# Optimization experiments

Measured on AMD Instinct MI355X. Metric: run time of the kernel, lower is better.

## Reference

```python
import jax, jax.numpy as jnp
import numpy as np

AGENT, WIN = 6, 7

def _rel_pos_index(d, h, w):
    # same construction as the torch buffer `relative_position_index`
    coords = np.stack(np.meshgrid(np.arange(d), np.arange(h), np.arange(w), indexing='ij'))
    cf = coords.reshape(3, -1)                                   # [3, S]
    rc = (cf[:, :, None] - cf[:, None, :]).transpose(1, 2, 0).astype(np.int64)
    rc[:, :, 0] += d - 1; rc[:, :, 1] += h - 1; rc[:, :, 2] += w - 1
    rc[:, :, 0] *= (2 * h - 1) * (2 * w - 1)
    rc[:, :, 1] *= (2 * w - 1)
    return jnp.asarray(rc.sum(-1))                               # [S, S]

def setup_inputs() -> dict:
    key = jax.random.key(0)
    ks = jax.random.split(key, 11)
    b, L, X, Y, w1, w2, dim = 2, AGENT, 8, 8, WIN, WIN, 256
    heads, ch, nt = 8, 32, 2
    table = (2 * L - 1) * (2 * w1 - 1) * (2 * w2 - 1)
    f = lambda k, s: (0.02 * jax.random.normal(k, s)).astype(jnp.float32)
    return dict(
        x=jax.random.normal(ks[0], (b, L, X, Y, w1, w2, dim), jnp.float32),
        Wq=f(ks[1], (nt, dim, dim)), bq=f(ks[2], (nt, dim)),
        Wk=f(ks[3], (nt, dim, dim)), bk=f(ks[4], (nt, dim)),
        Wv=f(ks[5], (nt, dim, dim)), bv=f(ks[6], (nt, dim)),
        rel_att=f(ks[7], (nt * nt, heads, ch, ch)),
        rel_msg=f(ks[8], (nt * nt, heads, ch, ch)),
        bias_table=f(ks[9], (table, heads)),
        Wo=f(ks[10], (dim, dim)),
        agent_type=1,
    )

def reference(x, Wq, bq, Wk, bk, Wv, bv, rel_att, rel_msg, bias_table, Wo, agent_type):
    b, L, X, Y, w1, w2, dim = x.shape
    heads, ch = rel_att.shape[1], rel_att.shape[2]
    nt = Wq.shape[0]
    scale = ch ** -0.5
    # types = [0] + (agent_size-1)*[type], identical across batch (as in forward)
    types = jnp.concatenate([jnp.zeros(1, jnp.int32),
                             jnp.full((L - 1,), agent_type, jnp.int32)])

    def proj(W, bias):
        # type-indexed per-agent linear (gathered batched matmul instead of python loops)
        y = jnp.einsum('blxyuvd,lde->blxyuve', x, W[types])
        y = y + bias[types][None, :, None, None, None, None, :]
        # -> [b, n=(X*Y) windows, m heads, L agents, p=(w1*w2) tokens, c]
        return y.reshape(b, L, X * Y, w1 * w2, heads, ch).transpose(0, 2, 4, 1, 3, 5)

    q = proj(Wq, bq) * scale
    k = proj(Wk, bk)
    v = proj(Wv, bv)

    # relation weights gathered by (src_type, dst_type) pair: [m, L, L, c, c]
    rel = types[:, None] * nt + types[None, :]
    w_att = rel_att[rel].transpose(2, 0, 1, 3, 4)
    w_msg = rel_msg[rel].transpose(2, 0, 1, 3, 4)

    # bilinear hetero attention scores, grouped by agent pair (i,j)
    sim = jnp.einsum('bnmipc,mijcf,bnmjqf->bnmipjq', q, w_att, k)
    S, n = L * w1 * w2, X * Y
    sim = sim.reshape(b, n, heads, S, S)
    idx = _rel_pos_index(L, w1, w2)                                # [S, S] static
    sim = sim + bias_table[idx].transpose(2, 0, 1)                 # + [m, S, S] rel-pos bias
    attn = jax.nn.softmax(sim, axis=-1).reshape(b, n, heads, L, w1 * w2, L, w1 * w2)

    # relation-transformed messages, then attention-weighted aggregation
    vt = jnp.einsum('mijcf,bnmjqf->bnmijqc', w_msg, v)
    out = jnp.einsum('bnmipjq,bnmijqc->bnmipc', attn, vt)
    # [b, n, m, L, p, c] -> [b, L, X, Y, w1, w2, dim]
    out = out.transpose(0, 3, 1, 4, 2, 5).reshape(b, L, X, Y, w1, w2, dim)
    return out @ Wo.T
```

## Files before the change

kernel.cpp:

```cpp
#include <hip/hip_runtime.h>
#include <hip/hip_bf16.h>

typedef __hip_bfloat16 bf16;
typedef unsigned short u16;
typedef short bf16x8 __attribute__((ext_vector_type(8)));
typedef float f32x4  __attribute__((ext_vector_type(4)));

#define BB    2
#define LL    6
#define NWIN  64
#define PP    49
#define DIMM  256
#define HEADS 8
#define CHN   32
#define SS    294
#define ASTRIDE 264
#define BSTRIDE 304
#define VST 328
#define PST 168

__device__ __forceinline__ u16 bfbits(float x) { return __bfloat16_as_ushort(__float2bfloat16(x)); }
__device__ __forceinline__ f32x4 mfma16(bf16x8 a, bf16x8 b, f32x4 c) {
    return __builtin_amdgcn_mfma_f32_16x16x32_bf16(a, b, c, 0, 0, 0);
}

__global__ __launch_bounds__(256) void k_prep(
    const float* __restrict__ Wq, const float* __restrict__ Wk, const float* __restrict__ Wv,
    const float* __restrict__ Wo, const float* __restrict__ ra, const float* __restrict__ rm,
    const float* __restrict__ bt,
    u16* __restrict__ wT, u16* __restrict__ Wob, u16* __restrict__ raT, u16* __restrict__ rmb,
    float* __restrict__ biasM)
{
    const int blk = blockIdx.x;
    if (blk < 1792) {
        const int idx = blk*256 + threadIdx.x;
        if (idx >= 7*65536) return;
        const int mat = idx >> 16, rem = idx & 65535;
        if (mat < 6) {
            const int tz = mat >> 1, t = mat & 1;
            const int e = rem >> 8, d = rem & 255;
            const float* W = (tz == 0 ? Wq : tz == 1 ? Wk : Wv);
            wT[mat*65536 + rem] = bfbits(W[t*65536 + d*256 + e]);
        } else {
            Wob[rem] = bfbits(Wo[rem]);
        }
    } else if (blk < 1920) {
        const int idx = (blk - 1792)*256 + threadIdx.x;
        if (idx < 4*HEADS*CHN*CHN) {
            const int pm = idx >> 10, cf = idx & 1023, c = cf >> 5, f = cf & 31;
            raT[(pm << 10) + (f << 5) + c] = bfbits(ra[idx]);
            rmb[idx] = bfbits(rm[idx]);
        }
    } else {
        const int idx = (blk - 1920)*256 + threadIdx.x;
        if (idx < HEADS*SS*BSTRIDE) {
            const int m = idx / (SS*BSTRIDE);
            const int rem = idx % (SS*BSTRIDE);
            const int s1 = rem / BSTRIDE, s2 = rem % BSTRIDE;
            float val = 0.f;
            if (s2 < SS) {
                const int i1 = s1/49, p1 = s1 - i1*49, h1 = p1/7, w1 = p1 - h1*7;
                const int j2 = s2/49, p2 = s2 - j2*49, h2 = p2/7, w2 = p2 - h2*7;
                const int rc = i1*169 + h1*13 + w1, cc = j2*169 + h2*13 + w2;
                val = bt[(rc - cc + 929)*8 + m];
            }
            biasM[idx] = val;
        }
    }
}

__global__ __launch_bounds__(256) void k_qkv2(
    const float* __restrict__ x, const u16* __restrict__ wT,
    const float* __restrict__ bq, const float* __restrict__ bk, const float* __restrict__ bv,
    const int* __restrict__ atype,
    u16* __restrict__ q, u16* __restrict__ k, u16* __restrict__ v)
{
    __shared__ __align__(16) u16 As[64*ASTRIDE];
    const int tid = threadIdx.x;
    const int w = tid >> 6, lane = tid & 63;
    const int g4 = lane >> 4, c16 = lane & 15;
    const int bid3 = blockIdx.x;
    const int tz = bid3 % 3;
    const int bid = bid3 / 3;
    const int nwin = bid & 63;
    const int l = (bid >> 6) % LL;
    const int b = bid / (LL*NWIN);

    const float4* xp = (const float4*)(x + (size_t)bid * (PP*DIMM));
    for (int idx = tid; idx < 49*64; idx += 256) {
        const int row = idx >> 6, c4 = idx & 63;
        const float4 xv = xp[idx];
        ushort4 h;
        h.x = bfbits(xv.x); h.y = bfbits(xv.y); h.z = bfbits(xv.z); h.w = bfbits(xv.w);
        *(ushort4*)&As[row*ASTRIDE + c4*4] = h;
    }
    const ushort4 z4 = {0, 0, 0, 0};
    for (int idx = tid; idx < 15*66; idx += 256) {
        const int row = 49 + idx/66, c4 = idx%66;
        *(ushort4*)&As[row*ASTRIDE + c4*4] = z4;
    }
    __syncthreads();

    const int t = (l == 0) ? 0 : atype[0];
    const f32x4 zero4 = {0.f, 0.f, 0.f, 0.f};

    const u16* WT = wT + (size_t)(tz*2 + t)*65536;
    const float* bias = (tz == 0 ? bq : tz == 1 ? bk : bv) + t*DIMM;
    u16* dst = (tz == 0 ? q : tz == 1 ? k : v);
    const float scale = (tz == 0) ? 0.17677669529663687f : 1.0f;

    f32x4 acc[4][4];
    #pragma unroll
    for (int mm = 0; mm < 4; ++mm)
        #pragma unroll
        for (int nn = 0; nn < 4; ++nn) acc[mm][nn] = zero4;

    for (int ks = 0; ks < 8; ++ks) {
        bf16x8 a[4], bb[4];
        #pragma unroll
        for (int mm = 0; mm < 4; ++mm)
            a[mm] = *(const bf16x8*)&As[(mm*16 + c16)*ASTRIDE + ks*32 + g4*8];
        #pragma unroll
        for (int nn = 0; nn < 4; ++nn)
            bb[nn] = *(const bf16x8*)&WT[(size_t)(w*64 + nn*16 + c16)*256 + ks*32 + g4*8];
        #pragma unroll
        for (int mm = 0; mm < 4; ++mm)
            #pragma unroll
            for (int nn = 0; nn < 4; ++nn)
                acc[mm][nn] = mfma16(a[mm], bb[nn], acc[mm][nn]);
    }

    #pragma unroll
    for (int nn = 0; nn < 4; ++nn) {
        const int col = w*64 + nn*16 + c16;
        const float bval = bias[col];
        const int head = col >> 5, c = col & 31;
        const size_t base = (((size_t)(b*NWIN + nwin)*HEADS + head)*SS + l*PP)*CHN + c;
        #pragma unroll
        for (int mm = 0; mm < 4; ++mm) {
            #pragma unroll
            for (int r = 0; r < 4; ++r) {
                const int row = mm*16 + g4*4 + r;
                if (row < PP)
                    dst[base + (size_t)row*CHN] = bfbits((acc[mm][nn][r] + bval)*scale);
            }
        }
    }
}

__global__ __launch_bounds__(256) void k_attn(
    const u16* __restrict__ q, const u16* __restrict__ kk_, const u16* __restrict__ v,
    const u16* __restrict__ raT, const u16* __restrict__ rmb,
    const float* __restrict__ biasM, const int* __restrict__ atype,
    u16* __restrict__ o_pre)
{
    __shared__ __align__(16) u16 vT[32*VST];
    __shared__ __align__(16) u16 vT0[32*72];
    __shared__ __align__(16) u16 wbuf[4*16*PST];

    const int tid  = threadIdx.x;
    const int w    = tid >> 6;
    const int lane = tid & 63;
    const int g4   = lane >> 4;
    const int c16  = lane & 15;
    const int bid  = blockIdx.x;
    const int m    = bid & 7;
    const int nwin = (bid >> 3) & 63;
    const int b    = bid >> 9;
    const int at   = atype[0];

    const size_t slab = (size_t)bid * (SS*CHN);
    const u16* qs  = q   + slab;
    const u16* ksg = kk_ + slab;
    const u16* vsg = v   + slab;
    const float* bm = biasM + (size_t)m*(SS*BSTRIDE);

    u16* wb = wbuf + w*(16*PST);

    for (int idx = tid; idx < 32*(VST - SS); idx += 256)
        vT[(idx/(VST - SS))*VST + SS + (idx%(VST - SS))] = 0;
    for (int idx = tid; idx < 32*15; idx += 256) vT0[(idx/15)*72 + 49 + (idx%15)] = 0;
    for (int idx = tid; idx < SS*CHN/2; idx += 256) {
        const int s2 = idx >> 4;
        const int f2 = (idx & 15) << 1;
        const unsigned int val = *(const unsigned int*)(vsg + s2*CHN + f2);
        const u16 v0 = (u16)(val & 0xffff), v1 = (u16)(val >> 16);
        vT[f2*VST + s2]     = v0;
        vT[(f2+1)*VST + s2] = v1;
        if (s2 < 49) { vT0[f2*72 + s2] = v0; vT0[(f2+1)*72 + s2] = v1; }
    }
    __syncthreads();

    const f32x4 zero4 = {0.f, 0.f, 0.f, 0.f};

    for (int job = w; job < 20; job += 4) {
        const int tile = (job == 19) ? 3 : job;
        const int tiv  = (job <= 3) ? 0 : at;
        const int pair0 = tiv*2;
        const int pair1 = tiv*2 + at;

        const int rowA = tile*16 + c16;
        const bf16x8 aq = *(const bf16x8*)(qs + rowA*CHN + g4*8);
        {
            const u16* base0 = raT + (pair0*HEADS + m)*1024;
            const u16* base1 = raT + (pair1*HEADS + m)*1024;
            const bf16x8 b00 = *(const bf16x8*)(base0 + (c16     )*32 + g4*8);
            const bf16x8 b01 = *(const bf16x8*)(base0 + (16 + c16)*32 + g4*8);
            const bf16x8 b10 = *(const bf16x8*)(base1 + (c16     )*32 + g4*8);
            const bf16x8 b11 = *(const bf16x8*)(base1 + (16 + c16)*32 + g4*8);
            const f32x4 cqw00 = mfma16(aq, b00, zero4);
            const f32x4 cqw01 = mfma16(aq, b01, zero4);
            const f32x4 cqw10 = mfma16(aq, b10, zero4);
            const f32x4 cqw11 = mfma16(aq, b11, zero4);
            #pragma unroll
            for (int r = 0; r < 4; ++r) {
                const int row = g4*4 + r;
                wb[row*72 +      c16] = bfbits(cqw00[r]);
                wb[row*72 + 16 + c16] = bfbits(cqw01[r]);
                wb[row*72 + 32 + c16] = bfbits(cqw10[r]);
                wb[row*72 + 48 + c16] = bfbits(cqw11[r]);
            }
        }
        const bf16x8 A0 = *(const bf16x8*)(wb + c16*72 +      g4*8);
        const bf16x8 A1 = *(const bf16x8*)(wb + c16*72 + 32 + g4*8);

        f32x4 acc[19];
        #pragma unroll
        for (int t = 0; t < 3; ++t) {
            const bf16x8 bk = *(const bf16x8*)(ksg + (t*16 + c16)*CHN + g4*8);
            acc[t] = mfma16(A0, bk, zero4);
        }
        {
            const bf16x8 bk = *(const bf16x8*)(ksg + (3*16 + c16)*CHN + g4*8);
            const f32x4 cA = mfma16(A0, bk, zero4);
            const f32x4 cB = mfma16(A1, bk, zero4);
            #pragma unroll
            for (int r = 0; r < 4; ++r) acc[3][r] = (c16 == 0) ? cA[r] : cB[r];
        }
        #pragma unroll
        for (int t = 4; t < 19; ++t) {
            const bf16x8 bk = *(const bf16x8*)(ksg + (t*16 + c16)*CHN + g4*8);
            acc[t] = mfma16(A1, bk, zero4);
        }

        const float* bmrow[4];
        #pragma unroll
        for (int r = 0; r < 4; ++r) {
            const int s1r = tile*16 + g4*4 + r;
            const int s1c = (s1r < SS) ? s1r : 293;
            bmrow[r] = bm + (size_t)s1c*BSTRIDE;
        }
        #pragma unroll
        for (int t = 0; t < 19; ++t)
            #pragma unroll
            for (int r = 0; r < 4; ++r)
                acc[t][r] += bmrow[r][t*16 + c16];
        #pragma unroll
        for (int r = 0; r < 4; ++r)
            acc[18][r] = (c16 < 6) ? acc[18][r] : -1e30f;

        float mx[4], sm[4];
        #pragma unroll
        for (int r = 0; r < 4; ++r) mx[r] = -1e30f;
        #pragma unroll
        for (int t = 0; t < 19; ++t)
            #pragma unroll
            for (int r = 0; r < 4; ++r) mx[r] = fmaxf(mx[r], acc[t][r]);
        #pragma unroll
        for (int off = 1; off < 16; off <<= 1)
            #pragma unroll
            for (int r = 0; r < 4; ++r) mx[r] = fmaxf(mx[r], __shfl_xor(mx[r], off));
        #pragma unroll
        for (int r = 0; r < 4; ++r) sm[r] = 0.f;
        #pragma unroll
        for (int t = 0; t < 19; ++t)
            #pragma unroll
            for (int r = 0; r < 4; ++r) { const float e = __expf(acc[t][r] - mx[r]); acc[t][r] = e; sm[r] += e; }
        #pragma unroll
        for (int off = 1; off < 16; off <<= 1)
            #pragma unroll
            for (int r = 0; r < 4; ++r) sm[r] += __shfl_xor(sm[r], off);
        #pragma unroll
        for (int r = 0; r < 4; ++r) {
            const float inv = 1.0f / sm[r];
            #pragma unroll
            for (int t = 0; t < 19; ++t) acc[t][r] *= inv;
        }

        f32x4 aggF0a = zero4, aggF0b = zero4, aggF1a = zero4, aggF1b = zero4;
        f32x4 agg00 = zero4, agg01 = zero4;
        bf16x8 asave0, asave1;
        #pragma unroll
        for (int t = 0; t < 10; ++t)
            #pragma unroll
            for (int r = 0; r < 4; ++r)
                wb[(g4*4 + r)*PST + t*16 + c16] = bfbits(acc[t][r]);
        #pragma unroll
        for (int ks = 0; ks < 5; ++ks) {
            const bf16x8 ap  = *(const bf16x8*)(wb + c16*PST + ks*32 + g4*8);
            const bf16x8 bv0 = *(const bf16x8*)(vT + (c16     )*VST + ks*32 + g4*8);
            const bf16x8 bv1 = *(const bf16x8*)(vT + (16 + c16)*VST + ks*32 + g4*8);
            if (ks & 1) { aggF0b = mfma16(ap, bv0, aggF0b); aggF1b = mfma16(ap, bv1, aggF1b); }
            else        { aggF0a = mfma16(ap, bv0, aggF0a); aggF1a = mfma16(ap, bv1, aggF1a); }
            if (ks == 0) asave0 = ap;
            if (ks == 1) asave1 = ap;
        }

        #pragma unroll
        for (int t2 = 0; t2 < 9; ++t2)
            #pragma unroll
            for (int r = 0; r < 4; ++r)
                wb[(g4*4 + r)*PST + t2*16 + c16] = bfbits(acc[10 + t2][r]);
        #pragma unroll
        for (int r = 0; r < 4; ++r)
            wb[(g4*4 + r)*PST + 9*16 + c16] = 0;
        #pragma unroll
        for (int ks2 = 0; ks2 < 5; ++ks2) {
            const int ks = 5 + ks2;
            const bf16x8 ap  = *(const bf16x8*)(wb + c16*PST + ks2*32 + g4*8);
            const bf16x8 bv0 = *(const bf16x8*)(vT + (c16     )*VST + ks*32 + g4*8);
            const bf16x8 bv1 = *(const bf16x8*)(vT + (16 + c16)*VST + ks*32 + g4*8);
            if (ks2 & 1) { aggF0b = mfma16(ap, bv0, aggF0b); aggF1b = mfma16(ap, bv1, aggF1b); }
            else         { aggF0a = mfma16(ap, bv0, aggF0a); aggF1a = mfma16(ap, bv1, aggF1a); }
        }

        {
            const bf16x8 b00 = *(const bf16x8*)(vT0 + (c16     )*72 +      g4*8);
            const bf16x8 b01 = *(const bf16x8*)(vT0 + (16 + c16)*72 +      g4*8);
            const bf16x8 b10 = *(const bf16x8*)(vT0 + (c16     )*72 + 32 + g4*8);
            const bf16x8 b11 = *(const bf16x8*)(vT0 + (16 + c16)*72 + 32 + g4*8);
            agg00 = mfma16(asave0, b00, agg00); agg00 = mfma16(asave1, b10, agg00);
            agg01 = mfma16(asave0, b01, agg01); agg01 = mfma16(asave1, b11, agg01);
        }
        const f32x4 aggF0 = aggF0a + aggF0b;
        const f32x4 aggF1 = aggF1a + aggF1b;
        const f32x4 agg10 = aggF0 - agg00;
        const f32x4 agg11 = aggF1 - agg01;

        #pragma unroll
        for (int r = 0; r < 4; ++r) {
            const int row = g4*4 + r;
            wb[row*72 +      c16] = bfbits(agg00[r]);
            wb[row*72 + 16 + c16] = bfbits(agg01[r]);
            wb[row*72 + 32 + c16] = bfbits(agg10[r]);
            wb[row*72 + 48 + c16] = bfbits(agg11[r]);
        }
        const bf16x8 aA0 = *(const bf16x8*)(wb + c16*72 +      g4*8);
        const bf16x8 aA1 = *(const bf16x8*)(wb + c16*72 + 32 + g4*8);
        const u16* mb0 = rmb + (pair0*HEADS + m)*1024;
        const u16* mb1 = rmb + (pair1*HEADS + m)*1024;
        const bf16x8 bm00 = *(const bf16x8*)(mb0 + (c16     )*32 + g4*8);
        const bf16x8 bm01 = *(const bf16x8*)(mb0 + (16 + c16)*32 + g4*8);
        const bf16x8 bm10 = *(const bf16x8*)(mb1 + (c16     )*32 + g4*8);
        const bf16x8 bm11 = *(const bf16x8*)(mb1 + (16 + c16)*32 + g4*8);
        f32x4 out0 = mfma16(aA0, bm00, zero4); out0 = mfma16(aA1, bm10, out0);
        f32x4 out1 = mfma16(aA0, bm01, zero4); out1 = mfma16(aA1, bm11, out1);

        #pragma unroll
        for (int r = 0; r < 4; ++r) {
            const int s1row = tile*16 + g4*4 + r;
            bool valid = (s1row < SS);
            if (job == 3)  valid = valid && (s1row == 48);
            if (job == 19) valid = valid && (s1row >= 49);
            if (valid) {
                const int i = s1row / 49, p = s1row - i*49;
                const size_t rb = ((size_t)((b*LL + i)*NWIN + nwin)*PP + p)*DIMM + m*CHN;
                o_pre[rb + c16]      = bfbits(out0[r]);
                o_pre[rb + 16 + c16] = bfbits(out1[r]);
            }
        }
    }
}

__global__ __launch_bounds__(256) void k_out2(
    const u16* __restrict__ pre, const u16* __restrict__ Wob,
    float* __restrict__ out)
{
    const int tid = threadIdx.x;
    const int w = tid >> 6, lane = tid & 63;
    const int g4 = lane >> 4, c16 = lane & 15;
    const int bid = blockIdx.x;
    const u16* ps = pre + (size_t)bid * (PP*DIMM);

    int rowc[4];
    #pragma unroll
    for (int mm = 0; mm < 4; ++mm) {
        const int r0 = mm*16 + c16;
        rowc[mm] = (r0 < PP) ? r0 : (PP - 1);
    }

    const f32x4 zero4 = {0.f, 0.f, 0.f, 0.f};
    f32x4 acc[4][4];
    #pragma unroll
    for (int mm = 0; mm < 4; ++mm)
        #pragma unroll
        for (int nn = 0; nn < 4; ++nn) acc[mm][nn] = zero4;

    for (int ks = 0; ks < 8; ++ks) {
        bf16x8 a[4], bb[4];
        #pragma unroll
        for (int mm = 0; mm < 4; ++mm)
            a[mm] = *(const bf16x8*)(ps + (size_t)rowc[mm]*DIMM + ks*32 + g4*8);
        #pragma unroll
        for (int nn = 0; nn < 4; ++nn)
            bb[nn] = *(const bf16x8*)&Wob[(size_t)(w*64 + nn*16 + c16)*256 + ks*32 + g4*8];
        #pragma unroll
        for (int mm = 0; mm < 4; ++mm)
            #pragma unroll
            for (int nn = 0; nn < 4; ++nn)
                acc[mm][nn] = mfma16(a[mm], bb[nn], acc[mm][nn]);
    }

    float* op = out + (size_t)bid * (PP*DIMM);
    #pragma unroll
    for (int nn = 0; nn < 4; ++nn) {
        const int col = w*64 + nn*16 + c16;
        #pragma unroll
        for (int mm = 0; mm < 4; ++mm) {
            #pragma unroll
            for (int r = 0; r < 4; ++r) {
                const int row = mm*16 + g4*4 + r;
                if (row < PP) op[(size_t)row*DIMM + col] = acc[mm][nn][r];
            }
        }
    }
}

extern "C" void kernel_launch(void* const* d_in, const int* in_sizes, int n_in,
                              void* d_out, int out_size, void* d_ws, size_t ws_size,
                              hipStream_t stream)
{
    (void)in_sizes; (void)n_in; (void)out_size; (void)ws_size;
    const float* x        = (const float*)d_in[0];
    const float* Wq       = (const float*)d_in[1];
    const float* bq       = (const float*)d_in[2];
    const float* Wk       = (const float*)d_in[3];
    const float* bk       = (const float*)d_in[4];
    const float* Wv       = (const float*)d_in[5];
    const float* bv       = (const float*)d_in[6];
    const float* rel_att  = (const float*)d_in[7];
    const float* rel_msg  = (const float*)d_in[8];
    const float* bias_tab = (const float*)d_in[9];
    const float* Wo       = (const float*)d_in[10];
    const int*   atype    = (const int*)d_in[11];
    float* out = (float*)d_out;

    char* ws = (char*)d_ws;
    u16* wT     = (u16*)ws;
    u16* Wob    = (u16*)(ws + 786432);
    u16* raT    = (u16*)(ws + 917504);
    u16* rmb    = (u16*)(ws + 983040);
    float* biasM= (float*)(ws + 1048576);
    u16* qb     = (u16*)(ws + 3908608);
    u16* kb     = (u16*)(ws + 3908608 + 1ull*19267584);
    u16* vb     = (u16*)(ws + 3908608 + 2ull*19267584);
    u16* o_preb = (u16*)(ws + 3908608 + 3ull*19267584);

    k_prep<<<4713, 256, 0, stream>>>(Wq, Wk, Wv, Wo, rel_att, rel_msg, bias_tab,
                                     wT, Wob, raT, rmb, biasM);
    k_qkv2<<<3*BB*LL*NWIN, 256, 0, stream>>>(x, wT, bq, bk, bv, atype, qb, kb, vb);
    k_attn<<<BB*NWIN*HEADS, 256, 0, stream>>>(qb, kb, vb, raT, rmb, biasM, atype, o_preb);
    k_out2<<<BB*LL*NWIN, 256, 0, stream>>>(o_preb, Wob, out);
}
```

Measured before the change: 223.9 us.

## Pre-convert x to swizzled bf16 once and tile-transpose weights in prep

Measured after the change: 222.6 us. About the same (-0.6%).

```diff
diff --git a/kernel.cpp b/kernel.cpp
--- a/kernel.cpp
+++ b/kernel.cpp
@@ -14,12 +14,14 @@
 #define HEADS 8
 #define CHN   32
 #define SS    294
-#define ASTRIDE 264
 #define BSTRIDE 304
 #define VST 328
 #define PST 168
 
 __device__ __forceinline__ u16 bfbits(float x) { return __bfloat16_as_ushort(__float2bfloat16(x)); }
+__device__ __forceinline__ unsigned int pk2(float a, float b) {
+    return (unsigned int)bfbits(a) | ((unsigned int)bfbits(b) << 16);
+}
 __device__ __forceinline__ f32x4 mfma16(bf16x8 a, bf16x8 b, f32x4 c) {
     return __builtin_amdgcn_mfma_f32_16x16x32_bf16(a, b, c, 0, 0, 0);
 }
@@ -27,32 +29,36 @@
 __global__ __launch_bounds__(256) void k_prep(
     const float* __restrict__ Wq, const float* __restrict__ Wk, const float* __restrict__ Wv,
     const float* __restrict__ Wo, const float* __restrict__ ra, const float* __restrict__ rm,
-    const float* __restrict__ bt,
+    const float* __restrict__ bt, const float* __restrict__ x,
     u16* __restrict__ wT, u16* __restrict__ Wob, u16* __restrict__ raT, u16* __restrict__ rmb,
-    float* __restrict__ biasM)
+    float* __restrict__ biasM, u16* __restrict__ xb)
 {
     const int blk = blockIdx.x;
-    if (blk < 1792) {
-        const int idx = blk*256 + threadIdx.x;
-        if (idx >= 7*65536) return;
-        const int mat = idx >> 16, rem = idx & 65535;
-        if (mat < 6) {
-            const int tz = mat >> 1, t = mat & 1;
-            const int e = rem >> 8, d = rem & 255;
-            const float* W = (tz == 0 ? Wq : tz == 1 ? Wk : Wv);
-            wT[mat*65536 + rem] = bfbits(W[t*65536 + d*256 + e]);
-        } else {
-            Wob[rem] = bfbits(Wo[rem]);
-        }
-    } else if (blk < 1920) {
-        const int idx = (blk - 1792)*256 + threadIdx.x;
-        if (idx < 4*HEADS*CHN*CHN) {
-            const int pm = idx >> 10, cf = idx & 1023, c = cf >> 5, f = cf & 31;
-            raT[(pm << 10) + (f << 5) + c] = bfbits(ra[idx]);
-            rmb[idx] = bfbits(rm[idx]);
-        }
-    } else {
-        const int idx = (blk - 1920)*256 + threadIdx.x;
+    const int tid = threadIdx.x;
+    if (blk < 384) {
+        __shared__ float tle[32][33];
+        const int mat = blk >> 6, tile = blk & 63;
+        const int bx = tile & 7, by = tile >> 3;
+        const int tx = tid & 31, ty = tid >> 5;
+        const int tz = mat >> 1, t = mat & 1;
+        const float* W = (tz == 0 ? Wq : tz == 1 ? Wk : Wv) + t*65536;
+        #pragma unroll
+        for (int r = 0; r < 32; r += 8)
+            tle[ty + r][tx] = W[(by*32 + ty + r)*256 + bx*32 + tx];
+        __syncthreads();
+        #pragma unroll
+        for (int r = 0; r < 32; r += 8)
+            wT[mat*65536 + (bx*32 + ty + r)*256 + by*32 + tx] = bfbits(tle[tx][ty + r]);
+    } else if (blk < 640) {
+        const int idx = (blk - 384)*256 + tid;
+        Wob[idx] = bfbits(Wo[idx]);
+    } else if (blk < 768) {
+        const int idx = (blk - 640)*256 + tid;
+        const int pm = idx >> 10, cf = idx & 1023, c = cf >> 5, f = cf & 31;
+        raT[(pm << 10) + (f << 5) + c] = bfbits(ra[idx]);
+        rmb[idx] = bfbits(rm[idx]);
+    } else if (blk < 3561) {
+        const int idx = (blk - 768)*256 + tid;
         if (idx < HEADS*SS*BSTRIDE) {
             const int m = idx / (SS*BSTRIDE);
             const int rem = idx % (SS*BSTRIDE);
@@ -66,16 +72,30 @@
             }
             biasM[idx] = val;
         }
+    } else {
+        const int idx = (blk - 3561)*256 + tid;
+        const int grp  = idx & 31;
+        const int row  = (idx >> 5) & 63;
+        const int slab = idx >> 11;
+        uint4 o = make_uint4(0u, 0u, 0u, 0u);
+        if (row < PP) {
+            const float* s = x + (size_t)slab*(PP*DIMM) + row*DIMM + ((grp ^ (row & 7)) << 3);
+            const float4 a = *(const float4*)s;
+            const float4 c = *(const float4*)(s + 4);
+            o.x = pk2(a.x, a.y); o.y = pk2(a.z, a.w);
+            o.z = pk2(c.x, c.y); o.w = pk2(c.z, c.w);
+        }
+        *(uint4*)(xb + (size_t)slab*16384 + row*256 + grp*8) = o;
     }
 }
 
 __global__ __launch_bounds__(256) void k_qkv2(
-    const float* __restrict__ x, const u16* __restrict__ wT,
+    const u16* __restrict__ xb, const u16* __restrict__ wT,
     const float* __restrict__ bq, const float* __restrict__ bk, const float* __restrict__ bv,
     const int* __restrict__ atype,
     u16* __restrict__ q, u16* __restrict__ k, u16* __restrict__ v)
 {
-    __shared__ __align__(16) u16 As[64*ASTRIDE];
+    __shared__ __align__(16) u16 As[64*256];
     const int tid = threadIdx.x;
     const int w = tid >> 6, lane = tid & 63;
     const int g4 = lane >> 4, c16 = lane & 15;
@@ -86,19 +106,9 @@
     const int l = (bid >> 6) % LL;
     const int b = bid / (LL*NWIN);
 
-    const float4* xp = (const float4*)(x + (size_t)bid * (PP*DIMM));
-    for (int idx = tid; idx < 49*64; idx += 256) {
-        const int row = idx >> 6, c4 = idx & 63;
-        const float4 xv = xp[idx];
-        ushort4 h;
-        h.x = bfbits(xv.x); h.y = bfbits(xv.y); h.z = bfbits(xv.z); h.w = bfbits(xv.w);
-        *(ushort4*)&As[row*ASTRIDE + c4*4] = h;
-    }
-    const ushort4 z4 = {0, 0, 0, 0};
-    for (int idx = tid; idx < 15*66; idx += 256) {
-        const int row = 49 + idx/66, c4 = idx%66;
-        *(ushort4*)&As[row*ASTRIDE + c4*4] = z4;
-    }
+    const uint4* src = (const uint4*)(xb + (size_t)bid*16384);
+    for (int j = tid; j < 2048; j += 256)
+        ((uint4*)As)[j] = src[j];
     __syncthreads();
 
     const int t = (l == 0) ? 0 : atype[0];
@@ -118,8 +128,10 @@
     for (int ks = 0; ks < 8; ++ks) {
         bf16x8 a[4], bb[4];
         #pragma unroll
-        for (int mm = 0; mm < 4; ++mm)
-            a[mm] = *(const bf16x8*)&As[(mm*16 + c16)*ASTRIDE + ks*32 + g4*8];
+        for (int mm = 0; mm < 4; ++mm) {
+            const int row = mm*16 + c16;
+            a[mm] = *(const bf16x8*)&As[row*256 + ((ks*32 + g4*8) ^ ((row & 7) << 3))];
+        }
         #pragma unroll
         for (int nn = 0; nn < 4; ++nn)
             bb[nn] = *(const bf16x8*)&WT[(size_t)(w*64 + nn*16 + c16)*256 + ks*32 + g4*8];
@@ -454,11 +466,12 @@
     u16* qb     = (u16*)(ws + 3908608);
     u16* kb     = (u16*)(ws + 3908608 + 1ull*19267584);
     u16* vb     = (u16*)(ws + 3908608 + 2ull*19267584);
-    u16* o_preb = (u16*)(ws + 3908608 + 3ull*19267584);
-
-    k_prep<<<4713, 256, 0, stream>>>(Wq, Wk, Wv, Wo, rel_att, rel_msg, bias_tab,
-                                     wT, Wob, raT, rmb, biasM);
-    k_qkv2<<<3*BB*LL*NWIN, 256, 0, stream>>>(x, wT, bq, bk, bv, atype, qb, kb, vb);
+    u16* o_preb = (u16*)(ws + 61711360);
+    u16* xb     = (u16*)(ws + 61711360);
+
+    k_prep<<<9705, 256, 0, stream>>>(Wq, Wk, Wv, Wo, rel_att, rel_msg, bias_tab, x,
+                                     wT, Wob, raT, rmb, biasM, xb);
+    k_qkv2<<<3*BB*LL*NWIN, 256, 0, stream>>>(xb, wT, bq, bk, bv, atype, qb, kb, vb);
     k_attn<<<BB*NWIN*HEADS, 256, 0, stream>>>(qb, kb, vb, raT, rmb, biasM, atype, o_preb);
     k_out2<<<BB*LL*NWIN, 256, 0, stream>>>(o_preb, Wob, out);
 }
```
